# Optimization experiments

Measured on AMD Instinct MI355X. Metric: run time of the kernel, lower is better.

## Reference

```python
import jax, jax.numpy as jnp
import numpy as np

EPS = 1e-9


def _pairwise_sqdist(x1, x2):
    # x1: (B,n,3), x2: (B,m,3) -> (B,n,m) squared euclidean distances
    s1 = jnp.sum(x1 * x1, axis=-1)
    s2 = jnp.sum(x2 * x2, axis=-1)
    cross = jnp.einsum('bnd,bmd->bnm', x1, x2)
    return jnp.maximum(s1[:, :, None] + s2[:, None, :] - 2.0 * cross, 0.0)


def _approxmatch(x1, x2):
    # Faithful port of the approxmatch CUDA kernel (Fan et al. EMD approx).
    B, n, _ = x1.shape
    m = x2.shape[1]
    if n >= m:
        multiL, multiR = 1.0, float(n // m)   # integer division as in CUDA
    else:
        multiL, multiR = float(m // n), 1.0
    dist = _pairwise_sqdist(x1, x2)  # (B,n,m)
    # j = 7 .. -1 -> level = -4^j ; j = -2 -> level = 0  (10 sweeps total)
    levels = jnp.concatenate([
        -(4.0 ** jnp.arange(7, -2, -1, dtype=jnp.float32)),
        jnp.zeros((1,), jnp.float32)])
    match0 = jnp.zeros((B, n, m), jnp.float32)
    remainL0 = jnp.full((B, n), multiL, jnp.float32)
    remainR0 = jnp.full((B, m), multiR, jnp.float32)

    def body(carry, level):
        match, remainL, remainR = carry
        e = jnp.exp(level * dist)                              # (B,n,m)
        suml = EPS + jnp.einsum('bnm,bm->bn', e, remainR)
        ratioL = remainL / suml                                # (B,n)
        sumr = remainR * jnp.einsum('bnm,bn->bm', e, ratioL)   # (B,m)
        consumption = jnp.minimum(remainR / (sumr + EPS), 1.0)
        ratioR = consumption * remainR                         # (B,m)
        remainR = jnp.maximum(0.0, remainR - sumr)
        w = e * ratioL[:, :, None] * ratioR[:, None, :]        # flow k->l
        match = match + w
        remainL = jnp.maximum(0.0, remainL - jnp.sum(w, axis=-1))
        return (match, remainL, remainR), None

    (match, _, _), _ = jax.lax.scan(body, (match0, remainL0, remainR0), levels)
    return match, dist


def setup_inputs() -> dict:
    key = jax.random.key(0)
    k1, k2 = jax.random.split(key)
    B, N = 4, 4096
    xyz1 = jax.random.normal(k1, (B, 3, N), dtype=jnp.float32)
    xyz2 = jax.random.normal(k2, (B, 3, N), dtype=jnp.float32)
    return {"xyz1": xyz1, "xyz2": xyz2}


def reference(xyz1, xyz2):
    # transpose=True: BCN -> BNC
    x1 = jnp.transpose(xyz1, (0, 2, 1))
    x2 = jnp.transpose(xyz2, (0, 2, 1))
    match, dist = _approxmatch(x1, x2)
    d = jnp.sqrt(jnp.maximum(dist, 1e-20))
    cost = jnp.sum(match * d, axis=(1, 2))            # (B,)
    emd = cost / min(x1.shape[1], x2.shape[1])
    return jnp.mean(emd)                               # reduce_mean=True
```

## Files before the change

kernel.cpp:

```cpp
#include <hip/hip_runtime.h>


#define NPTS 4096
#define BATCH 4
#define EMD_EPS 1e-9f
#define TILE 1024
#define RPW 4
#define THREADS 256
#define RPB 16
#define NBLK (NPTS / RPB)

#define CULL_FULL -160.0f
#define CULL_PART -40.0f

typedef float v2f __attribute__((ext_vector_type(2)));

__device__ __forceinline__ float fexp2(float x) {
#if __has_builtin(__builtin_amdgcn_exp2f)
    return __builtin_amdgcn_exp2f(x);
#else
    return exp2f(x);
#endif
}
__device__ __forceinline__ float fsqrt(float x) {
#if __has_builtin(__builtin_amdgcn_sqrtf)
    return __builtin_amdgcn_sqrtf(x);
#else
    return __sqrtf(x);
#endif
}

__device__ __forceinline__ float wave_reduce(float v) {
    v += __shfl_xor(v, 32);
    v += __shfl_xor(v, 16);
    v += __shfl_xor(v, 8);
    v += __shfl_xor(v, 4);
    v += __shfl_xor(v, 2);
    v += __shfl_xor(v, 1);
    return v;
}

__global__ __launch_bounds__(THREADS, 4) void k_ratioL0(
        const float* __restrict__ xyz1, const float* __restrict__ xyz2,
        float* __restrict__ ratioL, float* __restrict__ remainL,
        float* __restrict__ remainR, float ls2) {
    const int b = blockIdx.y;
    const int tid = threadIdx.x;
    const int wave = tid >> 6;
    const int lane = tid & 63;
    const int row0 = blockIdx.x * RPB + wave * RPW;

    const float* x1 = xyz1 + b * 3 * NPTS;
    const float* x2 = xyz2 + b * 3 * NPTS;
    const float2* x2x = (const float2*)(x2);
    const float2* x2y = (const float2*)(x2 + NPTS);
    const float2* x2z = (const float2*)(x2 + 2 * NPTS);

    float px[RPW], py[RPW], pz[RPW];
    v2f acc[RPW];
#pragma unroll
    for (int r = 0; r < RPW; ++r) {
        px[r] = x1[row0 + r];
        py[r] = x1[NPTS + row0 + r];
        pz[r] = x1[2 * NPTS + row0 + r];
        acc[r] = (v2f)(0.0f);
    }
    __shared__ float4 sA[TILE / 2];
    __shared__ float2 sZ[TILE / 2];

    for (int c0 = 0; c0 < NPTS; c0 += TILE) {
        __syncthreads();
        for (int i = tid; i < TILE / 2; i += THREADS) {
            int e = c0 / 2 + i;
            float2 xx = x2x[e], yy = x2y[e];
            sA[i] = make_float4(xx.x, xx.y, yy.x, yy.y);
            sZ[i] = x2z[e];
        }
        __syncthreads();
#pragma unroll 2
        for (int j = 0; j < TILE / 128; ++j) {
            float4 a = sA[lane + 64 * j];
            float2 z = sZ[lane + 64 * j];
            v2f ax = {a.x, a.y}, ay = {a.z, a.w}, az = {z.x, z.y};
#pragma unroll
            for (int r = 0; r < RPW; ++r) {
                v2f dx = px[r] - ax, dy = py[r] - ay, dz = pz[r] - az;
                v2f d = dx * dx + dy * dy + dz * dz;
                v2f sd = ls2 * d;
                if (!__all(fmaxf(sd.x, sd.y) < CULL_FULL)) {
                    v2f e2 = {fexp2(sd.x), fexp2(sd.y)};
                    acc[r] += e2;
                }
            }
        }
    }
#pragma unroll
    for (int r = 0; r < RPW; ++r) {
        float s = wave_reduce(acc[r].x + acc[r].y);
        if (lane == 0) {
            int idx = b * NPTS + row0 + r;
            ratioL[idx] = 1.0f / (EMD_EPS + s);
            remainL[idx] = 1.0f;
            remainR[idx] = 1.0f;
        }
    }
}

template <bool CULL>
__global__ __launch_bounds__(THREADS, 4) void k_ratioR(
        const float* __restrict__ xyz1, const float* __restrict__ xyz2,
        const float* __restrict__ ratioL, float* __restrict__ ratioR,
        float* __restrict__ remainR, float ls2) {
    const int b = blockIdx.y;
    const int tid = threadIdx.x;
    const int wave = tid >> 6;
    const int lane = tid & 63;
    const int col0 = blockIdx.x * RPB + wave * RPW;

    const float* x1 = xyz1 + b * 3 * NPTS;
    const float* x2 = xyz2 + b * 3 * NPTS;
    const float2* x1x = (const float2*)(x1);
    const float2* x1y = (const float2*)(x1 + NPTS);
    const float2* x1z = (const float2*)(x1 + 2 * NPTS);
    const float2* wLv = (const float2*)(ratioL + b * NPTS);

    float px[RPW], py[RPW], pz[RPW];
    v2f acc[RPW];
#pragma unroll
    for (int r = 0; r < RPW; ++r) {
        px[r] = x2[col0 + r];
        py[r] = x2[NPTS + col0 + r];
        pz[r] = x2[2 * NPTS + col0 + r];
        acc[r] = (v2f)(0.0f);
    }
    __shared__ float4 sA[TILE / 2];
    __shared__ float4 sB[TILE / 2];

    for (int c0 = 0; c0 < NPTS; c0 += TILE) {
        __syncthreads();
        for (int i = tid; i < TILE / 2; i += THREADS) {
            int e = c0 / 2 + i;
            float2 xx = x1x[e], yy = x1y[e], zz = x1z[e], ww = wLv[e];
            sA[i] = make_float4(xx.x, xx.y, yy.x, yy.y);
            sB[i] = make_float4(zz.x, zz.y, ww.x, ww.y);
        }
        __syncthreads();
#pragma unroll 2
        for (int j = 0; j < TILE / 128; ++j) {
            float4 a = sA[lane + 64 * j];
            float4 bq = sB[lane + 64 * j];
            v2f ax = {a.x, a.y}, ay = {a.z, a.w};
            v2f az = {bq.x, bq.y}, aw = {bq.z, bq.w};
#pragma unroll
            for (int r = 0; r < RPW; ++r) {
                v2f dx = px[r] - ax, dy = py[r] - ay, dz = pz[r] - az;
                v2f d = dx * dx + dy * dy + dz * dz;
                v2f sd = ls2 * d;
                bool live = true;
                if (CULL) live = !__all(fmaxf(sd.x, sd.y) < CULL_FULL);
                if (live) {
                    v2f e2 = {fexp2(sd.x), fexp2(sd.y)};
                    acc[r] += e2 * aw;
                }
            }
        }
    }
#pragma unroll
    for (int r = 0; r < RPW; ++r) {
        float s = wave_reduce(acc[r].x + acc[r].y);
        if (lane == 0) {
            int idx = b * NPTS + col0 + r;
            float rv = remainR[idx];
            float sumr = rv * s;
            float cons = fminf(rv / (sumr + EMD_EPS), 1.0f);
            ratioR[idx] = cons * rv;
            remainR[idx] = fmaxf(0.0f, rv - sumr);
        }
    }
}

template <bool SQ, bool CULL>
__global__ __launch_bounds__(THREADS, 4) void k_cost_fused(
        const float* __restrict__ xyz1, const float* __restrict__ xyz2,
        float* __restrict__ ratioL, const float* __restrict__ ratioR,
        float* __restrict__ remainL, const float* __restrict__ remainR,
        float* __restrict__ cost_part, float ls2, float ls2n, int initCost) {
    const int b = blockIdx.y;
    const int tid = threadIdx.x;
    const int wave = tid >> 6;
    const int lane = tid & 63;
    const int row0 = blockIdx.x * RPB + wave * RPW;

    const float* x1 = xyz1 + b * 3 * NPTS;
    const float* x2 = xyz2 + b * 3 * NPTS;
    const float2* x2x = (const float2*)(x2);
    const float2* x2y = (const float2*)(x2 + NPTS);
    const float2* x2z = (const float2*)(x2 + 2 * NPTS);
    const float2* wRv = (const float2*)(ratioR + b * NPTS);
    const float2* w2v = (const float2*)(remainR + b * NPTS);

    float px[RPW], py[RPW], pz[RPW];
    v2f acc_a[RPW], acc_c[RPW], acc_s[RPW];
#pragma unroll
    for (int r = 0; r < RPW; ++r) {
        px[r] = x1[row0 + r];
        py[r] = x1[NPTS + row0 + r];
        pz[r] = x1[2 * NPTS + row0 + r];
        acc_a[r] = (v2f)(0.0f);
        acc_c[r] = (v2f)(0.0f);
        acc_s[r] = (v2f)(0.0f);
    }
    __shared__ float4 sA[TILE / 2];
    __shared__ float4 sB[TILE / 2];
    __shared__ float2 sC[TILE / 2];
    __shared__ float s_cost[THREADS / 64];

    for (int c0 = 0; c0 < NPTS; c0 += TILE) {
        __syncthreads();
        for (int i = tid; i < TILE / 2; i += THREADS) {
            int e = c0 / 2 + i;
            float2 xx = x2x[e], yy = x2y[e], zz = x2z[e], wr = wRv[e];
            sA[i] = make_float4(xx.x, xx.y, yy.x, yy.y);
            sB[i] = make_float4(zz.x, zz.y, wr.x, wr.y);
            sC[i] = w2v[e];
        }
        __syncthreads();
#pragma unroll 2
        for (int j = 0; j < TILE / 128; ++j) {
            float4 a = sA[lane + 64 * j];
            float4 bq = sB[lane + 64 * j];
            float2 c = sC[lane + 64 * j];
            v2f ax = {a.x, a.y}, ay = {a.z, a.w};
            v2f az = {bq.x, bq.y}, wr = {bq.z, bq.w};
            v2f cw = {c.x, c.y};
#pragma unroll
            for (int r = 0; r < RPW; ++r) {
                v2f dx = px[r] - ax, dy = py[r] - ay, dz = pz[r] - az;
                v2f d = dx * dx + dy * dy + dz * dz;
                if (SQ) {
                    v2f sd = ls2n * d;
                    bool fullskip = false, partskip = false;
                    if (CULL) {
                        float mx = fmaxf(sd.x, sd.y);
                        fullskip = __all(mx < CULL_FULL);
                        partskip = __all(mx < CULL_PART);
                    }
                    if (!fullskip) {
                        v2f e2 = {fexp2(sd.x), fexp2(sd.y)};
                        acc_s[r] += e2 * cw;
                        if (!partskip) {
                            v2f e4 = e2 * e2;
                            v2f er = (e4 * e4) * wr;
                            acc_a[r] += er;
                            v2f sq = {fsqrt(d.x), fsqrt(d.y)};
                            acc_c[r] += er * sq;
                        }
                    }
                } else {
                    v2f sd = ls2 * d;
                    v2f e1 = {fexp2(sd.x), fexp2(sd.y)};
                    v2f er = e1 * wr;
                    acc_s[r] += cw;
                    acc_a[r] += er;
                    v2f sq = {fsqrt(d.x), fsqrt(d.y)};
                    acc_c[r] += er * sq;
                }
            }
        }
    }
    float wcost = 0.0f;
#pragma unroll
    for (int r = 0; r < RPW; ++r) {
        float sa = wave_reduce(acc_a[r].x + acc_a[r].y);
        float sc = wave_reduce(acc_c[r].x + acc_c[r].y);
        float ss = wave_reduce(acc_s[r].x + acc_s[r].y);
        if (lane == 0) {
            int idx = b * NPTS + row0 + r;
            float rl = ratioL[idx];
            float rem = fmaxf(0.0f, remainL[idx] - rl * sa);
            remainL[idx] = rem;
            ratioL[idx] = rem / (EMD_EPS + ss);
            wcost = fmaf(rl, sc, wcost);
        }
    }
    if (lane == 0) s_cost[wave] = wcost;
    __syncthreads();
    if (tid == 0) {
        float t = s_cost[0] + s_cost[1] + s_cost[2] + s_cost[3];
        int ci = b * NBLK + blockIdx.x;
        cost_part[ci] = (initCost ? t : cost_part[ci] + t);
    }
}

__global__ void k_sum_ratioL(const float* __restrict__ ratioL, float* __restrict__ S_L) {
    const int b = blockIdx.x;
    const int tid = threadIdx.x;
    float s = 0.0f;
    for (int i = tid; i < NPTS; i += 256) s += ratioL[b * NPTS + i];
    s = wave_reduce(s);
    __shared__ float sw[4];
    if ((tid & 63) == 0) sw[tid >> 6] = s;
    __syncthreads();
    if (tid == 0) S_L[b] = sw[0] + sw[1] + sw[2] + sw[3];
}

__global__ __launch_bounds__(THREADS, 4) void k_cost_l0(
        const float* __restrict__ xyz1, const float* __restrict__ xyz2,
        const float* __restrict__ ratioL, const float* __restrict__ remainR,
        const float* __restrict__ S_L, float* __restrict__ cost_part) {
    const int b = blockIdx.y;
    const int tid = threadIdx.x;
    const int wave = tid >> 6;
    const int lane = tid & 63;
    const int row0 = blockIdx.x * RPB + wave * RPW;
    const float sL = S_L[b];

    const float* x1 = xyz1 + b * 3 * NPTS;
    const float* x2 = xyz2 + b * 3 * NPTS;
    const float2* x2x = (const float2*)(x2);
    const float2* x2y = (const float2*)(x2 + NPTS);
    const float2* x2z = (const float2*)(x2 + 2 * NPTS);
    const float2* wRv = (const float2*)(remainR + b * NPTS);

    float px[RPW], py[RPW], pz[RPW];
    v2f acc_c[RPW];
#pragma unroll
    for (int r = 0; r < RPW; ++r) {
        px[r] = x1[row0 + r];
        py[r] = x1[NPTS + row0 + r];
        pz[r] = x1[2 * NPTS + row0 + r];
        acc_c[r] = (v2f)(0.0f);
    }
    __shared__ float4 sA[TILE / 2];
    __shared__ float4 sB[TILE / 2];
    __shared__ float s_cost[THREADS / 64];

    for (int c0 = 0; c0 < NPTS; c0 += TILE) {
        __syncthreads();
        for (int i = tid; i < TILE / 2; i += THREADS) {
            int e = c0 / 2 + i;
            float2 xx = x2x[e], yy = x2y[e], zz = x2z[e], rv = wRv[e];
            float wr0 = fminf(rv.x / (rv.x * sL + EMD_EPS), 1.0f) * rv.x;
            float wr1 = fminf(rv.y / (rv.y * sL + EMD_EPS), 1.0f) * rv.y;
            sA[i] = make_float4(xx.x, xx.y, yy.x, yy.y);
            sB[i] = make_float4(zz.x, zz.y, wr0, wr1);
        }
        __syncthreads();
#pragma unroll 2
        for (int j = 0; j < TILE / 128; ++j) {
            float4 a = sA[lane + 64 * j];
            float4 bq = sB[lane + 64 * j];
            v2f ax = {a.x, a.y}, ay = {a.z, a.w};
            v2f az = {bq.x, bq.y}, wr = {bq.z, bq.w};
#pragma unroll
            for (int r = 0; r < RPW; ++r) {
                v2f dx = px[r] - ax, dy = py[r] - ay, dz = pz[r] - az;
                v2f d = dx * dx + dy * dy + dz * dz;
                v2f sq = {fsqrt(d.x), fsqrt(d.y)};
                acc_c[r] += wr * sq;
            }
        }
    }
    float wcost = 0.0f;
#pragma unroll
    for (int r = 0; r < RPW; ++r) {
        float sc = wave_reduce(acc_c[r].x + acc_c[r].y);
        if (lane == 0)
            wcost = fmaf(ratioL[b * NPTS + row0 + r], sc, wcost);
    }
    if (lane == 0) s_cost[wave] = wcost;
    __syncthreads();
    if (tid == 0) {
        float t = s_cost[0] + s_cost[1] + s_cost[2] + s_cost[3];
        cost_part[b * NBLK + blockIdx.x] += t;
    }
}

__global__ void k_final(const float* __restrict__ cost_part, float* __restrict__ out) {
    const int tid = threadIdx.x;
    float s = 0.0f;
    for (int i = tid; i < BATCH * NBLK; i += 256) s += cost_part[i];
    s = wave_reduce(s);
    __shared__ float sw[4];
    if ((tid & 63) == 0) sw[tid >> 6] = s;
    __syncthreads();
    if (tid == 0) out[0] = (sw[0] + sw[1] + sw[2] + sw[3]) / ((float)NPTS * (float)BATCH);
}

extern "C" void kernel_launch(void* const* d_in, const int* in_sizes, int n_in,
                              void* d_out, int out_size, void* d_ws, size_t ws_size,
                              hipStream_t stream) {
    const float* xyz1 = (const float*)d_in[0];
    const float* xyz2 = (const float*)d_in[1];
    float* out = (float*)d_out;

    const int BN = BATCH * NPTS;
    float* ws = (float*)d_ws;
    float* remainL  = ws;
    float* remainR  = ws + 1 * BN;
    float* ratioL   = ws + 2 * BN;
    float* ratioR   = ws + 3 * BN;
    float* cost_part = ws + 4 * BN;
    float* S_L      = cost_part + BATCH * NBLK;

    static const float levels[10] = {
        -16384.0f, -4096.0f, -1024.0f, -256.0f, -64.0f,
        -16.0f, -4.0f, -1.0f, -0.25f, 0.0f};
    float ls2[10];
    for (int t = 0; t < 10; ++t)
        ls2[t] = (float)(levels[t] * 1.4426950408889634);

    dim3 grid(NBLK, BATCH);

    k_ratioL0<<<grid, THREADS, 0, stream>>>(xyz1, xyz2, ratioL, remainL, remainR, ls2[0]);
    for (int t = 0; t < 8; ++t) {
        if (t < 3) {
            k_ratioR<true><<<grid, THREADS, 0, stream>>>(xyz1, xyz2, ratioL, ratioR,
                                                         remainR, ls2[t]);
            k_cost_fused<true, true><<<grid, THREADS, 0, stream>>>(
                xyz1, xyz2, ratioL, ratioR, remainL, remainR, cost_part,
                ls2[t], ls2[t + 1], t == 0 ? 1 : 0);
        } else {
            k_ratioR<false><<<grid, THREADS, 0, stream>>>(xyz1, xyz2, ratioL, ratioR,
                                                          remainR, ls2[t]);
            k_cost_fused<true, false><<<grid, THREADS, 0, stream>>>(
                xyz1, xyz2, ratioL, ratioR, remainL, remainR, cost_part,
                ls2[t], ls2[t + 1], 0);
        }
    }
    k_ratioR<false><<<grid, THREADS, 0, stream>>>(xyz1, xyz2, ratioL, ratioR,
                                                  remainR, ls2[8]);
    k_cost_fused<false, false><<<grid, THREADS, 0, stream>>>(
        xyz1, xyz2, ratioL, ratioR, remainL, remainR, cost_part, ls2[8], 0.0f, 0);
    k_sum_ratioL<<<BATCH, 256, 0, stream>>>(ratioL, S_L);
    k_cost_l0<<<grid, THREADS, 0, stream>>>(xyz1, xyz2, ratioL, remainR, S_L, cost_part);
    k_final<<<1, 256, 0, stream>>>(cost_part, out);
}
```

Before: 527.5 us.

## Fuse all EMD phases into one cooperative persistent kernel with grid syncs

Replaces the roughly 22 separate kernel launches with a single cooperative kernel that runs every phase and separates them with grid-wide barriers, keeping the old multi-launch path as a fallback. Rows per wave are doubled (RPW 8, RPB 32), which halves the grid to 512 blocks so it can be co-resident, and launch bounds drop to 2 blocks per CU. This targets launch overhead and inter-kernel gaps, but it doubles register pressure per thread and halves parallelism per phase. Grid syncs also have a cost, and the cooperative launch may fail if the blocks do not fit on the device at once.

```diff
diff --git a/kernel.cpp b/kernel.cpp
--- a/kernel.cpp
+++ b/kernel.cpp
@@ -1,19 +1,42 @@
 #include <hip/hip_runtime.h>
+#include <hip/hip_cooperative_groups.h>
+
+namespace cg = cooperative_groups;
 
 
 #define NPTS 4096
 #define BATCH 4
 #define EMD_EPS 1e-9f
 #define TILE 1024
-#define RPW 4
+#define RPW 8
 #define THREADS 256
-#define RPB 16
+#define RPB 32
 #define NBLK (NPTS / RPB)
 
 #define CULL_FULL -160.0f
 #define CULL_PART -40.0f
 
 typedef float v2f __attribute__((ext_vector_type(2)));
+
+struct Params {
+    const float* xyz1;
+    const float* xyz2;
+    float* remainL;
+    float* remainR;
+    float* ratioL;
+    float* ratioR;
+    float* cost_part;
+    float* S_L;
+    float* out;
+    float ls2[10];
+};
+
+struct Smem {
+    float4 sA[TILE / 2];
+    float4 sB[TILE / 2];
+    float2 sC[TILE / 2];
+    float  s_cost[THREADS / 64];
+};
 
 __device__ __forceinline__ float fexp2(float x) {
 #if __has_builtin(__builtin_amdgcn_exp2f)
@@ -40,18 +63,15 @@
     return v;
 }
 
-__global__ __launch_bounds__(THREADS, 4) void k_ratioL0(
-        const float* __restrict__ xyz1, const float* __restrict__ xyz2,
-        float* __restrict__ ratioL, float* __restrict__ remainL,
-        float* __restrict__ remainR, float ls2) {
+__device__ __forceinline__ void phase_ratioL0(Smem& sm, const Params& p, float ls2) {
     const int b = blockIdx.y;
     const int tid = threadIdx.x;
     const int wave = tid >> 6;
     const int lane = tid & 63;
     const int row0 = blockIdx.x * RPB + wave * RPW;
 
-    const float* x1 = xyz1 + b * 3 * NPTS;
-    const float* x2 = xyz2 + b * 3 * NPTS;
+    const float* x1 = p.xyz1 + b * 3 * NPTS;
+    const float* x2 = p.xyz2 + b * 3 * NPTS;
     const float2* x2x = (const float2*)(x2);
     const float2* x2y = (const float2*)(x2 + NPTS);
     const float2* x2z = (const float2*)(x2 + 2 * NPTS);
@@ -65,22 +85,19 @@
         pz[r] = x1[2 * NPTS + row0 + r];
         acc[r] = (v2f)(0.0f);
     }
-    __shared__ float4 sA[TILE / 2];
-    __shared__ float2 sZ[TILE / 2];
-
     for (int c0 = 0; c0 < NPTS; c0 += TILE) {
         __syncthreads();
         for (int i = tid; i < TILE / 2; i += THREADS) {
             int e = c0 / 2 + i;
             float2 xx = x2x[e], yy = x2y[e];
-            sA[i] = make_float4(xx.x, xx.y, yy.x, yy.y);
-            sZ[i] = x2z[e];
+            sm.sA[i] = make_float4(xx.x, xx.y, yy.x, yy.y);
+            sm.sC[i] = x2z[e];
         }
         __syncthreads();
 #pragma unroll 2
         for (int j = 0; j < TILE / 128; ++j) {
-            float4 a = sA[lane + 64 * j];
-            float2 z = sZ[lane + 64 * j];
+            float4 a = sm.sA[lane + 64 * j];
+            float2 z = sm.sC[lane + 64 * j];
             v2f ax = {a.x, a.y}, ay = {a.z, a.w}, az = {z.x, z.y};
 #pragma unroll
             for (int r = 0; r < RPW; ++r) {
@@ -99,30 +116,27 @@
         float s = wave_reduce(acc[r].x + acc[r].y);
         if (lane == 0) {
             int idx = b * NPTS + row0 + r;
-            ratioL[idx] = 1.0f / (EMD_EPS + s);
-            remainL[idx] = 1.0f;
-            remainR[idx] = 1.0f;
+            p.ratioL[idx] = 1.0f / (EMD_EPS + s);
+            p.remainL[idx] = 1.0f;
+            p.remainR[idx] = 1.0f;
         }
     }
 }
 
 template <bool CULL>
-__global__ __launch_bounds__(THREADS, 4) void k_ratioR(
-        const float* __restrict__ xyz1, const float* __restrict__ xyz2,
-        const float* __restrict__ ratioL, float* __restrict__ ratioR,
-        float* __restrict__ remainR, float ls2) {
+__device__ __forceinline__ void phase_ratioR(Smem& sm, const Params& p, float ls2) {
     const int b = blockIdx.y;
     const int tid = threadIdx.x;
     const int wave = tid >> 6;
     const int lane = tid & 63;
     const int col0 = blockIdx.x * RPB + wave * RPW;
 
-    const float* x1 = xyz1 + b * 3 * NPTS;
-    const float* x2 = xyz2 + b * 3 * NPTS;
+    const float* x1 = p.xyz1 + b * 3 * NPTS;
+    const float* x2 = p.xyz2 + b * 3 * NPTS;
     const float2* x1x = (const float2*)(x1);
     const float2* x1y = (const float2*)(x1 + NPTS);
     const float2* x1z = (const float2*)(x1 + 2 * NPTS);
-    const float2* wLv = (const float2*)(ratioL + b * NPTS);
+    const float2* wLv = (const float2*)(p.ratioL + b * NPTS);
 
     float px[RPW], py[RPW], pz[RPW];
     v2f acc[RPW];
@@ -133,22 +147,19 @@
         pz[r] = x2[2 * NPTS + col0 + r];
         acc[r] = (v2f)(0.0f);
     }
-    __shared__ float4 sA[TILE / 2];
-    __shared__ float4 sB[TILE / 2];
-
     for (int c0 = 0; c0 < NPTS; c0 += TILE) {
         __syncthreads();
         for (int i = tid; i < TILE / 2; i += THREADS) {
             int e = c0 / 2 + i;
             float2 xx = x1x[e], yy = x1y[e], zz = x1z[e], ww = wLv[e];
-            sA[i] = make_float4(xx.x, xx.y, yy.x, yy.y);
-            sB[i] = make_float4(zz.x, zz.y, ww.x, ww.y);
+            sm.sA[i] = make_float4(xx.x, xx.y, yy.x, yy.y);
+            sm.sB[i] = make_float4(zz.x, zz.y, ww.x, ww.y);
         }
         __syncthreads();
 #pragma unroll 2
         for (int j = 0; j < TILE / 128; ++j) {
-            float4 a = sA[lane + 64 * j];
-            float4 bq = sB[lane + 64 * j];
+            float4 a = sm.sA[lane + 64 * j];
+            float4 bq = sm.sB[lane + 64 * j];
             v2f ax = {a.x, a.y}, ay = {a.z, a.w};
             v2f az = {bq.x, bq.y}, aw = {bq.z, bq.w};
 #pragma unroll
@@ -170,34 +181,31 @@
         float s = wave_reduce(acc[r].x + acc[r].y);
         if (lane == 0) {
             int idx = b * NPTS + col0 + r;
-            float rv = remainR[idx];
+            float rv = p.remainR[idx];
             float sumr = rv * s;
             float cons = fminf(rv / (sumr + EMD_EPS), 1.0f);
-            ratioR[idx] = cons * rv;
-            remainR[idx] = fmaxf(0.0f, rv - sumr);
+            p.ratioR[idx] = cons * rv;
+            p.remainR[idx] = fmaxf(0.0f, rv - sumr);
         }
     }
 }
 
 template <bool SQ, bool CULL>
-__global__ __launch_bounds__(THREADS, 4) void k_cost_fused(
-        const float* __restrict__ xyz1, const float* __restrict__ xyz2,
-        float* __restrict__ ratioL, const float* __restrict__ ratioR,
-        float* __restrict__ remainL, const float* __restrict__ remainR,
-        float* __restrict__ cost_part, float ls2, float ls2n, int initCost) {
+__device__ __forceinline__ void phase_cost(Smem& sm, const Params& p,
+                                           float ls2, float ls2n, int initCost) {
     const int b = blockIdx.y;
     const int tid = threadIdx.x;
     const int wave = tid >> 6;
     const int lane = tid & 63;
     const int row0 = blockIdx.x * RPB + wave * RPW;
 
-    const float* x1 = xyz1 + b * 3 * NPTS;
-    const float* x2 = xyz2 + b * 3 * NPTS;
+    const float* x1 = p.xyz1 + b * 3 * NPTS;
+    const float* x2 = p.xyz2 + b * 3 * NPTS;
     const float2* x2x = (const float2*)(x2);
     const float2* x2y = (const float2*)(x2 + NPTS);
     const float2* x2z = (const float2*)(x2 + 2 * NPTS);
-    const float2* wRv = (const float2*)(ratioR + b * NPTS);
-    const float2* w2v = (const float2*)(remainR + b * NPTS);
+    const float2* wRv = (const float2*)(p.ratioR + b * NPTS);
+    const float2* w2v = (const float2*)(p.remainR + b * NPTS);
 
     float px[RPW], py[RPW], pz[RPW];
     v2f acc_a[RPW], acc_c[RPW], acc_s[RPW];
@@ -210,26 +218,21 @@
         acc_c[r] = (v2f)(0.0f);
         acc_s[r] = (v2f)(0.0f);
     }
-    __shared__ float4 sA[TILE / 2];
-    __shared__ float4 sB[TILE / 2];
-    __shared__ float2 sC[TILE / 2];
-    __shared__ float s_cost[THREADS / 64];
-
     for (int c0 = 0; c0 < NPTS; c0 += TILE) {
         __syncthreads();
         for (int i = tid; i < TILE / 2; i += THREADS) {
             int e = c0 / 2 + i;
             float2 xx = x2x[e], yy = x2y[e], zz = x2z[e], wr = wRv[e];
-            sA[i] = make_float4(xx.x, xx.y, yy.x, yy.y);
-            sB[i] = make_float4(zz.x, zz.y, wr.x, wr.y);
-            sC[i] = w2v[e];
+            sm.sA[i] = make_float4(xx.x, xx.y, yy.x, yy.y);
+            sm.sB[i] = make_float4(zz.x, zz.y, wr.x, wr.y);
+            sm.sC[i] = w2v[e];
         }
         __syncthreads();
 #pragma unroll 2
         for (int j = 0; j < TILE / 128; ++j) {
-            float4 a = sA[lane + 64 * j];
-            float4 bq = sB[lane + 64 * j];
-            float2 c = sC[lane + 64 * j];
+            float4 a = sm.sA[lane + 64 * j];
+            float4 bq = sm.sB[lane + 64 * j];
+            float2 c = sm.sC[lane + 64 * j];
             v2f ax = {a.x, a.y}, ay = {a.z, a.w};
             v2f az = {bq.x, bq.y}, wr = {bq.z, bq.w};
             v2f cw = {c.x, c.y};
@@ -276,51 +279,48 @@
         float ss = wave_reduce(acc_s[r].x + acc_s[r].y);
         if (lane == 0) {
             int idx = b * NPTS + row0 + r;
-            float rl = ratioL[idx];
-            float rem = fmaxf(0.0f, remainL[idx] - rl * sa);
-            remainL[idx] = rem;
-            ratioL[idx] = rem / (EMD_EPS + ss);
+            float rl = p.ratioL[idx];
+            float rem = fmaxf(0.0f, p.remainL[idx] - rl * sa);
+            p.remainL[idx] = rem;
+            p.ratioL[idx] = rem / (EMD_EPS + ss);
             wcost = fmaf(rl, sc, wcost);
         }
     }
-    if (lane == 0) s_cost[wave] = wcost;
+    if (lane == 0) sm.s_cost[wave] = wcost;
     __syncthreads();
     if (tid == 0) {
-        float t = s_cost[0] + s_cost[1] + s_cost[2] + s_cost[3];
+        float t = sm.s_cost[0] + sm.s_cost[1] + sm.s_cost[2] + sm.s_cost[3];
         int ci = b * NBLK + blockIdx.x;
-        cost_part[ci] = (initCost ? t : cost_part[ci] + t);
-    }
-}
-
-__global__ void k_sum_ratioL(const float* __restrict__ ratioL, float* __restrict__ S_L) {
-    const int b = blockIdx.x;
+        p.cost_part[ci] = (initCost ? t : p.cost_part[ci] + t);
+    }
+}
+
+__device__ __forceinline__ void phase_sum_ratioL(Smem& sm, const Params& p) {
+    if (blockIdx.x != 0) return;
+    const int b = blockIdx.y;
     const int tid = threadIdx.x;
     float s = 0.0f;
-    for (int i = tid; i < NPTS; i += 256) s += ratioL[b * NPTS + i];
+    for (int i = tid; i < NPTS; i += 256) s += p.ratioL[b * NPTS + i];
     s = wave_reduce(s);
-    __shared__ float sw[4];
-    if ((tid & 63) == 0) sw[tid >> 6] = s;
+    if ((tid & 63) == 0) sm.s_cost[tid >> 6] = s;
     __syncthreads();
-    if (tid == 0) S_L[b] = sw[0] + sw[1] + sw[2] + sw[3];
-}
-
-__global__ __launch_bounds__(THREADS, 4) void k_cost_l0(
-        const float* __restrict__ xyz1, const float* __restrict__ xyz2,
-        const float* __restrict__ ratioL, const float* __restrict__ remainR,
-        const float* __restrict__ S_L, float* __restrict__ cost_part) {
+    if (tid == 0) p.S_L[b] = sm.s_cost[0] + sm.s_cost[1] + sm.s_cost[2] + sm.s_cost[3];
+}
+
+__device__ __forceinline__ void phase_cost_l0(Smem& sm, const Params& p) {
     const int b = blockIdx.y;
     const int tid = threadIdx.x;
     const int wave = tid >> 6;
     const int lane = tid & 63;
     const int row0 = blockIdx.x * RPB + wave * RPW;
-    const float sL = S_L[b];
-
-    const float* x1 = xyz1 + b * 3 * NPTS;
-    const float* x2 = xyz2 + b * 3 * NPTS;
+    const float sL = p.S_L[b];
+
+    const float* x1 = p.xyz1 + b * 3 * NPTS;
+    const float* x2 = p.xyz2 + b * 3 * NPTS;
     const float2* x2x = (const float2*)(x2);
     const float2* x2y = (const float2*)(x2 + NPTS);
     const float2* x2z = (const float2*)(x2 + 2 * NPTS);
-    const float2* wRv = (const float2*)(remainR + b * NPTS);
+    const float2* wRv = (const float2*)(p.remainR + b * NPTS);
 
     float px[RPW], py[RPW], pz[RPW];
     v2f acc_c[RPW];
@@ -331,10 +331,6 @@
         pz[r] = x1[2 * NPTS + row0 + r];
         acc_c[r] = (v2f)(0.0f);
     }
-    __shared__ float4 sA[TILE / 2];
-    __shared__ float4 sB[TILE / 2];
-    __shared__ float s_cost[THREADS / 64];
-
     for (int c0 = 0; c0 < NPTS; c0 += TILE) {
         __syncthreads();
         for (int i = tid; i < TILE / 2; i += THREADS) {
@@ -342,14 +338,14 @@
             float2 xx = x2x[e], yy = x2y[e], zz = x2z[e], rv = wRv[e];
             float wr0 = fminf(rv.x / (rv.x * sL + EMD_EPS), 1.0f) * rv.x;
             float wr1 = fminf(rv.y / (rv.y * sL + EMD_EPS), 1.0f) * rv.y;
-            sA[i] = make_float4(xx.x, xx.y, yy.x, yy.y);
-            sB[i] = make_float4(zz.x, zz.y, wr0, wr1);
+            sm.sA[i] = make_float4(xx.x, xx.y, yy.x, yy.y);
+            sm.sB[i] = make_float4(zz.x, zz.y, wr0, wr1);
         }
         __syncthreads();
 #pragma unroll 2
         for (int j = 0; j < TILE / 128; ++j) {
-            float4 a = sA[lane + 64 * j];
-            float4 bq = sB[lane + 64 * j];
+            float4 a = sm.sA[lane + 64 * j];
+            float4 bq = sm.sB[lane + 64 * j];
             v2f ax = {a.x, a.y}, ay = {a.z, a.w};
             v2f az = {bq.x, bq.y}, wr = {bq.z, bq.w};
 #pragma unroll
@@ -366,73 +362,123 @@
     for (int r = 0; r < RPW; ++r) {
         float sc = wave_reduce(acc_c[r].x + acc_c[r].y);
         if (lane == 0)
-            wcost = fmaf(ratioL[b * NPTS + row0 + r], sc, wcost);
-    }
-    if (lane == 0) s_cost[wave] = wcost;
+            wcost = fmaf(p.ratioL[b * NPTS + row0 + r], sc, wcost);
+    }
+    if (lane == 0) sm.s_cost[wave] = wcost;
     __syncthreads();
     if (tid == 0) {
-        float t = s_cost[0] + s_cost[1] + s_cost[2] + s_cost[3];
-        cost_part[b * NBLK + blockIdx.x] += t;
-    }
-}
-
-__global__ void k_final(const float* __restrict__ cost_part, float* __restrict__ out) {
+        float t = sm.s_cost[0] + sm.s_cost[1] + sm.s_cost[2] + sm.s_cost[3];
+        p.cost_part[b * NBLK + blockIdx.x] += t;
+    }
+}
+
+__device__ __forceinline__ void phase_final(Smem& sm, const Params& p) {
+    if (blockIdx.x != 0 || blockIdx.y != 0) return;
     const int tid = threadIdx.x;
     float s = 0.0f;
-    for (int i = tid; i < BATCH * NBLK; i += 256) s += cost_part[i];
+    for (int i = tid; i < BATCH * NBLK; i += 256) s += p.cost_part[i];
     s = wave_reduce(s);
-    __shared__ float sw[4];
-    if ((tid & 63) == 0) sw[tid >> 6] = s;
+    if ((tid & 63) == 0) sm.s_cost[tid >> 6] = s;
     __syncthreads();
-    if (tid == 0) out[0] = (sw[0] + sw[1] + sw[2] + sw[3]) / ((float)NPTS * (float)BATCH);
+    if (tid == 0)
+        p.out[0] = (sm.s_cost[0] + sm.s_cost[1] + sm.s_cost[2] + sm.s_cost[3]) /
+                   ((float)NPTS * (float)BATCH);
+}
+
+__global__ __launch_bounds__(THREADS, 2) void k_emd_all(Params p) {
+    cg::grid_group g = cg::this_grid();
+    __shared__ Smem sm;
+
+    phase_ratioL0(sm, p, p.ls2[0]);
+    g.sync();
+    for (int t = 0; t < 9; ++t) {
+        if (t < 3) phase_ratioR<true>(sm, p, p.ls2[t]);
+        else       phase_ratioR<false>(sm, p, p.ls2[t]);
+        g.sync();
+        if (t < 3)      phase_cost<true, true>(sm, p, p.ls2[t], p.ls2[t + 1], t == 0);
+        else if (t < 8) phase_cost<true, false>(sm, p, p.ls2[t], p.ls2[t + 1], 0);
+        else            phase_cost<false, false>(sm, p, p.ls2[8], 0.0f, 0);
+        g.sync();
+    }
+    phase_sum_ratioL(sm, p);
+    g.sync();
+    phase_cost_l0(sm, p);
+    g.sync();
+    phase_final(sm, p);
+}
+
+__global__ __launch_bounds__(THREADS, 2) void kw_ratioL0(Params p) {
+    __shared__ Smem sm;
+    phase_ratioL0(sm, p, p.ls2[0]);
+}
+__global__ __launch_bounds__(THREADS, 2) void kw_ratioR(Params p, int t) {
+    __shared__ Smem sm;
+    if (t < 3) phase_ratioR<true>(sm, p, p.ls2[t]);
+    else       phase_ratioR<false>(sm, p, p.ls2[t]);
+}
+__global__ __launch_bounds__(THREADS, 2) void kw_cost(Params p, int t) {
+    __shared__ Smem sm;
+    if (t < 3)      phase_cost<true, true>(sm, p, p.ls2[t], p.ls2[t + 1], t == 0);
+    else if (t < 8) phase_cost<true, false>(sm, p, p.ls2[t], p.ls2[t + 1], 0);
+    else            phase_cost<false, false>(sm, p, p.ls2[8], 0.0f, 0);
+}
+__global__ __launch_bounds__(THREADS, 2) void kw_sum(Params p) {
+    __shared__ Smem sm;
+    phase_sum_ratioL(sm, p);
+}
+__global__ __launch_bounds__(THREADS, 2) void kw_cost_l0(Params p) {
+    __shared__ Smem sm;
+    phase_cost_l0(sm, p);
+}
+__global__ __launch_bounds__(THREADS, 2) void kw_final(Params p) {
+    __shared__ Smem sm;
+    phase_final(sm, p);
 }
 
 extern "C" void kernel_launch(void* const* d_in, const int* in_sizes, int n_in,
                               void* d_out, int out_size, void* d_ws, size_t ws_size,
                               hipStream_t stream) {
-    const float* xyz1 = (const float*)d_in[0];
-    const float* xyz2 = (const float*)d_in[1];
-    float* out = (float*)d_out;
-
+    Params p;
+    p.xyz1 = (const float*)d_in[0];
+    p.xyz2 = (const float*)d_in[1];
     const int BN = BATCH * NPTS;
     float* ws = (float*)d_ws;
-    float* remainL  = ws;
-    float* remainR  = ws + 1 * BN;
-    float* ratioL   = ws + 2 * BN;
-    float* ratioR   = ws + 3 * BN;
-    float* cost_part = ws + 4 * BN;
-    float* S_L      = cost_part + BATCH * NBLK;
-
-    static const float levels[10] = {
-        -16384.0f, -4096.0f, -1024.0f, -256.0f, -64.0f,
-        -16.0f, -4.0f, -1.0f, -0.25f, 0.0f};
-    float ls2[10];
+    p.remainL   = ws;
+    p.remainR   = ws + 1 * BN;
+    p.ratioL    = ws + 2 * BN;
+    p.ratioR    = ws + 3 * BN;
+    p.cost_part = ws + 4 * BN;
+    p.S_L       = p.cost_part + BATCH * NBLK;
+    p.out       = (float*)d_out;
+
+    static const double levels[10] = {
+        -16384.0, -4096.0, -1024.0, -256.0, -64.0,
+        -16.0, -4.0, -1.0, -0.25, 0.0};
     for (int t = 0; t < 10; ++t)
-        ls2[t] = (float)(levels[t] * 1.4426950408889634);
-
-    dim3 grid(NBLK, BATCH);
-
-    k_ratioL0<<<grid, THREADS, 0, stream>>>(xyz1, xyz2, ratioL, remainL, remainR, ls2[0]);
-    for (int t = 0; t < 8; ++t) {
-        if (t < 3) {
-            k_ratioR<true><<<grid, THREADS, 0, stream>>>(xyz1, xyz2, ratioL, ratioR,
-                                                         remainR, ls2[t]);
-            k_cost_fused<true, true><<<grid, THREADS, 0, stream>>>(
-                xyz1, xyz2, ratioL, ratioR, remainL, remainR, cost_part,
-                ls2[t], ls2[t + 1], t == 0 ? 1 : 0);
-        } else {
-            k_ratioR<false><<<grid, THREADS, 0, stream>>>(xyz1, xyz2, ratioL, ratioR,
-                                                          remainR, ls2[t]);
-            k_cost_fused<true, false><<<grid, THREADS, 0, stream>>>(
-                xyz1, xyz2, ratioL, ratioR, remainL, remainR, cost_part,
-                ls2[t], ls2[t + 1], 0);
-        }
-    }
-    k_ratioR<false><<<grid, THREADS, 0, stream>>>(xyz1, xyz2, ratioL, ratioR,
-                                                  remainR, ls2[8]);
-    k_cost_fused<false, false><<<grid, THREADS, 0, stream>>>(
-        xyz1, xyz2, ratioL, ratioR, remainL, remainR, cost_part, ls2[8], 0.0f, 0);
-    k_sum_ratioL<<<BATCH, 256, 0, stream>>>(ratioL, S_L);
-    k_cost_l0<<<grid, THREADS, 0, stream>>>(xyz1, xyz2, ratioL, remainR, S_L, cost_part);
-    k_final<<<1, 256, 0, stream>>>(cost_part, out);
-}
+        p.ls2[t] = (float)(levels[t] * 1.4426950408889634);
+
+    dim3 grid(NBLK, BATCH), blk(THREADS);
+
+    static int coop_ok = -1;
+    if (coop_ok < 0) {
+        int v = 0;
+        hipDeviceGetAttribute(&v, hipDeviceAttributeCooperativeLaunch, 0);
+        coop_ok = v;
+    }
+
+    hipError_t err = hipErrorUnknown;
+    if (coop_ok) {
+        void* args[] = {(void*)&p};
+        err = hipLaunchCooperativeKernel((void*)k_emd_all, grid, blk, args, 0, stream);
+    }
+    if (err != hipSuccess) {
+        kw_ratioL0<<<grid, blk, 0, stream>>>(p);
+        for (int t = 0; t < 9; ++t) {
+            kw_ratioR<<<grid, blk, 0, stream>>>(p, t);
+            kw_cost<<<grid, blk, 0, stream>>>(p, t);
+        }
+        kw_sum<<<dim3(1, BATCH), blk, 0, stream>>>(p);
+        kw_cost_l0<<<grid, blk, 0, stream>>>(p);
+        kw_final<<<dim3(1, 1), blk, 0, stream>>>(p);
+    }
+}
```

New measurement: 1.940 ms. 3.68x slower.
